# Performance work log

Hardware: AMD Instinct MI355X
Metric: run time of the kernel (lower is better)

Reference implementation:

```python
import jax, jax.numpy as jnp
import numpy as np

B, T, C, D = 4, 2048, 1024, 64

def setup_inputs() -> dict:
    key = jax.random.key(0)
    ks = jax.random.split(key, 7)
    s = 1.0 / np.sqrt(C)
    return {
        "x":  jax.random.normal(ks[0], (B, T, C), dtype=jnp.float32),
        "Wq": jax.random.uniform(ks[1], (C, D), jnp.float32, -s, s),
        "bq": jax.random.uniform(ks[2], (D,),  jnp.float32, -s, s),
        "Wk": jax.random.uniform(ks[3], (C, D), jnp.float32, -s, s),
        "bk": jax.random.uniform(ks[4], (D,),  jnp.float32, -s, s),
        "Wv": jax.random.uniform(ks[5], (C, D), jnp.float32, -s, s),
        "bv": jax.random.uniform(ks[6], (D,),  jnp.float32, -s, s),
    }

def reference(x, Wq, bq, Wk, bk, Wv, bv):
    # QKV projections: [B,T,C] @ [C,D] -> [B,T,D]
    Q = jnp.einsum('btc,cd->btd', x, Wq) + bq
    K = jnp.einsum('btc,cd->btd', x, Wk) + bk
    V = jnp.einsum('btc,cd->btd', x, Wv) + bv
    scale = 1.0 / jnp.sqrt(jnp.float32(D))
    wei = jnp.einsum('bqd,bkd->bqk', Q, K) * scale  # [B,T,T]
    causal = jnp.tril(jnp.ones((T, T), dtype=bool))
    wei = jnp.where(causal, wei, jnp.float32(-1e9))  # masked_fill, not -inf
    wei = jax.nn.softmax(wei, axis=-1)
    return jnp.einsum('bqk,bkd->bqd', wei, V)  # [B,T,D]
```

## Files before the change

### kernel.cpp

```cpp
#include <hip/hip_runtime.h>
#include <stdint.h>

#define B_  4
#define T_  2048
#define C_  1024
#define D_  64

typedef float  f32x4  __attribute__((ext_vector_type(4)));
typedef float  f32x16 __attribute__((ext_vector_type(16)));
typedef short  s16x8  __attribute__((ext_vector_type(8)));

#define QSCALE 0.18033688011112042f

static __device__ __forceinline__ uint32_t f2bf(float f) {
  uint32_t u = __builtin_bit_cast(uint32_t, f);
  u += 0x7FFFu + ((u >> 16) & 1u);
  return u >> 16;
}
static __device__ __forceinline__ uint32_t pack2bf(float a, float b) {
  return f2bf(a) | (f2bf(b) << 16);
}

__global__ __launch_bounds__(256) void wconv_kernel(
    const float* __restrict__ Wq, const float* __restrict__ bq,
    const float* __restrict__ Wk, const float* __restrict__ bk,
    const float* __restrict__ Wv, const float* __restrict__ bv,
    uint16_t* __restrict__ Wp, float* __restrict__ biascat) {
  const int g = blockIdx.x * 256 + threadIdx.x;
  const int s32   = g / 768;
  const int rem   = g - s32 * 768;
  const int ntile = rem >> 6;
  const int l     = rem & 63;
  const int mrow  = l & 15, u = l >> 4;
  const int n     = ntile * 16 + mrow;
  const int mat   = n >> 6, col = n & 63;
  const float* W  = (mat == 0) ? Wq : ((mat == 1) ? Wk : Wv);
  const float  s  = (mat == 0) ? QSCALE : 1.0f;
  const int c0    = s32 * 32 + u * 8;
  float v[8];
#pragma unroll
  for (int j = 0; j < 8; ++j) v[j] = W[(size_t)(c0 + j) * D_ + col] * s;
  uint4 st;
  st.x = pack2bf(v[0], v[1]);
  st.y = pack2bf(v[2], v[3]);
  st.z = pack2bf(v[4], v[5]);
  st.w = pack2bf(v[6], v[7]);
  *reinterpret_cast<uint4*>(Wp + (size_t)g * 8) = st;
  if (g < 192) {
    float bb;
    if (g < 64)       bb = bq[g] * QSCALE;
    else if (g < 128) bb = bk[g - 64];
    else              bb = bv[g - 128];
    biascat[g] = bb;
  }
}

__global__ __launch_bounds__(512) void proj_kernel(
    const float* __restrict__ x, const uint16_t* __restrict__ Wp,
    const float* __restrict__ biascat,
    uint16_t* __restrict__ Qfrag, uint16_t* __restrict__ Kfrag,
    uint16_t* __restrict__ Vfrag) {
  __shared__ __align__(16) uint16_t xt[2][32 * 132];
  __shared__ __align__(16) uint16_t tbuf[8][16 * 28];
  const int tid   = threadIdx.x;
  const int wave  = tid >> 6;
  const int lane  = tid & 63;
  const int mrow  = lane & 15;
  const int u     = lane >> 4;
  const int wn    = wave & 3;
  const int mhalf = wave >> 2;
  const int m0    = blockIdx.x * 32;
  const int mw    = m0 + mhalf * 16;
  const int srow  = tid >> 4, scol = tid & 15;

  const float* xg = x + (size_t)(m0 + srow) * C_ + scol * 4;

  f32x4 acc[3];
#pragma unroll
  for (int i = 0; i < 3; ++i)
#pragma unroll
    for (int r = 0; r < 4; ++r) acc[i][r] = 0.f;

  float4 xv0 = *reinterpret_cast<const float4*>(xg);
  float4 xv1 = *reinterpret_cast<const float4*>(xg + 64);
  {
    uint2 w0, w1;
    w0.x = pack2bf(xv0.x, xv0.y);  w0.y = pack2bf(xv0.z, xv0.w);
    w1.x = pack2bf(xv1.x, xv1.y);  w1.y = pack2bf(xv1.z, xv1.w);
    *reinterpret_cast<uint2*>(&xt[0][srow * 132 + scol * 4])      = w0;
    *reinterpret_cast<uint2*>(&xt[0][srow * 132 + scol * 4 + 64]) = w1;
  }
  __syncthreads();

  for (int s = 0; s < 8; ++s) {
    const int cur = s & 1;
    if (s < 7) {
      xv0 = *reinterpret_cast<const float4*>(xg + (s + 1) * 128);
      xv1 = *reinterpret_cast<const float4*>(xg + (s + 1) * 128 + 64);
    }
#pragma unroll
    for (int step = 0; step < 4; ++step) {
      const int s32 = s * 4 + step;
      s16x8 bf = *reinterpret_cast<const s16x8*>(
          &xt[cur][(mhalf * 16 + mrow) * 132 + step * 32 + u * 8]);
      const uint16_t* wb = Wp + ((size_t)(s32 * 12 + wn * 3) * 64 + lane) * 8;
      s16x8 a0 = *reinterpret_cast<const s16x8*>(wb);
      s16x8 a1 = *reinterpret_cast<const s16x8*>(wb + 64 * 8);
      s16x8 a2 = *reinterpret_cast<const s16x8*>(wb + 128 * 8);
      acc[0] = __builtin_amdgcn_mfma_f32_16x16x32_bf16(a0, bf, acc[0], 0, 0, 0);
      acc[1] = __builtin_amdgcn_mfma_f32_16x16x32_bf16(a1, bf, acc[1], 0, 0, 0);
      acc[2] = __builtin_amdgcn_mfma_f32_16x16x32_bf16(a2, bf, acc[2], 0, 0, 0);
    }
    if (s < 7) {
      uint2 w0, w1;
      w0.x = pack2bf(xv0.x, xv0.y);  w0.y = pack2bf(xv0.z, xv0.w);
      w1.x = pack2bf(xv1.x, xv1.y);  w1.y = pack2bf(xv1.z, xv1.w);
      *reinterpret_cast<uint2*>(&xt[cur ^ 1][srow * 132 + scol * 4])      = w0;
      *reinterpret_cast<uint2*>(&xt[cur ^ 1][srow * 132 + scol * 4 + 64]) = w1;
      __syncthreads();
    }
  }

  const int bb = m0 >> 11;
  const int mm = mw & (T_ - 1);
#pragma unroll
  for (int nt = 0; nt < 3; ++nt) {
    const int nb = wn * 48 + nt * 16;
    uint16_t vals[4];
#pragma unroll
    for (int r = 0; r < 4; ++r)
      vals[r] = (uint16_t)f2bf(acc[nt][r] + biascat[nb + u * 4 + r]);
    if (nb >= 128) {
      const int tg  = mm + mrow;
      const int t   = tg >> 5, rem = tg & 31;
      const int kc  = rem >> 4, hi2 = (rem >> 3) & 1, jj = rem & 7;
      uint16_t* base = Vfrag + ((size_t)(bb * 64 + t)) * 2048;
#pragma unroll
      for (int r = 0; r < 4; ++r) {
        int d = nb - 128 + u * 4 + r;
        int i = (d >> 5) * 2 + kc;
        int l = hi2 * 32 + (d & 31);
        base[i * 512 + l * 8 + jj] = vals[r];
      }
    } else {
#pragma unroll
      for (int r = 0; r < 4; ++r)
        tbuf[wave][mrow * 28 + u * 4 + r] = vals[r];
      const int row = lane >> 2, qtr = lane & 3;
      uint2 v = *reinterpret_cast<const uint2*>(&tbuf[wave][row * 28 + qtr * 4]);
      const int m  = mw + row;
      const int e0 = (nb & 63) + qtr * 4;
      const int t  = (m & 2047) >> 5;
      const int c  = e0 >> 4, hi2 = (e0 >> 3) & 1, j0 = e0 & 7;
      uint16_t* dst = (nb < 64) ? Qfrag : Kfrag;
      *reinterpret_cast<uint2*>(
          dst + ((size_t)(bb * 64 + t)) * 2048 + c * 512 +
          (hi2 * 32 + (m & 31)) * 8 + j0) = v;
    }
  }
}

__global__ __launch_bounds__(512) void attn_kernel(
    const uint16_t* __restrict__ Qfrag, const uint16_t* __restrict__ Kfrag,
    const uint16_t* __restrict__ Vfrag, float* __restrict__ out) {
  __shared__ float wpart[8 * 2048];
  __shared__ float lw[8 * 32];
  __shared__ float lbuf[32];

  const int tid  = threadIdx.x;
  const int wave = tid >> 6;
  const int lane = tid & 63;
  const int ql   = lane & 31;
  const int hi   = lane >> 5;

  const int blk = blockIdx.x;
  const int b   = blk & 3;
  const int qt  = 63 - (blk >> 2);

  s16x8 qf[4];
  {
    const uint16_t* qg = Qfrag + ((size_t)(b * 64 + qt)) * 2048 + lane * 8;
#pragma unroll
    for (int c = 0; c < 4; ++c)
      qf[c] = *reinterpret_cast<const s16x8*>(qg + c * 512);
  }

  f32x16 aco[2];
#pragma unroll
  for (int i = 0; i < 2; ++i)
#pragma unroll
    for (int r = 0; r < 16; ++r) aco[i][r] = 0.f;
  float lacc = 0.f;

  auto load_tile = [&](int t, s16x8* kf, s16x8* vf) {
    const uint16_t* kg = Kfrag + ((size_t)(b * 64 + t)) * 2048 + lane * 8;
#pragma unroll
    for (int c = 0; c < 4; ++c)
      kf[c] = *reinterpret_cast<const s16x8*>(kg + c * 512);
    const uint16_t* vg = Vfrag + ((size_t)(b * 64 + t)) * 2048 + lane * 8;
#pragma unroll
    for (int i = 0; i < 4; ++i)
      vf[i] = *reinterpret_cast<const s16x8*>(vg + i * 512);
  };

  auto compute = [&](int t, const s16x8* kf, const s16x8* vf) {
    f32x16 sacc;
#pragma unroll
    for (int r = 0; r < 16; ++r) sacc[r] = 0.f;
#pragma unroll
    for (int c = 0; c < 4; ++c)
      sacc = __builtin_amdgcn_mfma_f32_32x32x16_bf16(kf[c], qf[c], sacc, 0, 0, 0);
    if (t == qt) {
#pragma unroll
      for (int r = 0; r < 16; ++r) {
        const int koff = (r & 3) + 8 * (r >> 2) + 4 * hi;
        sacc[r] = (koff > ql) ? -1e30f : sacc[r];
      }
    }
    float p[16];
#pragma unroll
    for (int r = 0; r < 16; ++r) p[r] = __builtin_amdgcn_exp2f(sacc[r]);
    float s01 = (p[0] + p[1]) + (p[2] + p[3]);
    float s23 = (p[4] + p[5]) + (p[6] + p[7]);
    float s45 = (p[8] + p[9]) + (p[10] + p[11]);
    float s67 = (p[12] + p[13]) + (p[14] + p[15]);
    lacc += (s01 + s23) + (s45 + s67);

    uint32_t A0 = pack2bf(p[0], p[1]),  A1 = pack2bf(p[2], p[3]);
    uint32_t B0 = pack2bf(p[4], p[5]),  B1 = pack2bf(p[6], p[7]);
    uint32_t C0 = pack2bf(p[8], p[9]),  C1 = pack2bf(p[10], p[11]);
    uint32_t D0 = pack2bf(p[12], p[13]), D1 = pack2bf(p[14], p[15]);
    uint32_t r0 = (uint32_t)__shfl_xor((int)(hi ? A0 : B0), 32, 64);
    uint32_t r1 = (uint32_t)__shfl_xor((int)(hi ? A1 : B1), 32, 64);
    uint32_t r2 = (uint32_t)__shfl_xor((int)(hi ? C0 : D0), 32, 64);
    uint32_t r3 = (uint32_t)__shfl_xor((int)(hi ? C1 : D1), 32, 64);
    union { uint32_t u[4]; s16x8 v; } pf0, pf1;
    pf0.u[0] = hi ? r0 : A0;  pf0.u[1] = hi ? r1 : A1;
    pf0.u[2] = hi ? B0 : r0;  pf0.u[3] = hi ? B1 : r1;
    pf1.u[0] = hi ? r2 : C0;  pf1.u[1] = hi ? r3 : C1;
    pf1.u[2] = hi ? D0 : r2;  pf1.u[3] = hi ? D1 : r3;
    aco[0] = __builtin_amdgcn_mfma_f32_32x32x16_bf16(vf[0], pf0.v, aco[0], 0, 0, 0);
    aco[1] = __builtin_amdgcn_mfma_f32_32x32x16_bf16(vf[2], pf0.v, aco[1], 0, 0, 0);
    aco[0] = __builtin_amdgcn_mfma_f32_32x32x16_bf16(vf[1], pf1.v, aco[0], 0, 0, 0);
    aco[1] = __builtin_amdgcn_mfma_f32_32x32x16_bf16(vf[3], pf1.v, aco[1], 0, 0, 0);
  };

  {
    int t = wave;
    if (t <= qt) {
      s16x8 kfA[4], vfA[4], kfB[4], vfB[4];
      load_tile(t, kfA, vfA);
      while (true) {
        int tn = t + 8;
        if (tn <= qt) load_tile(tn, kfB, vfB);
        compute(t, kfA, vfA);
        if (tn > qt) break;
        t = tn; tn = t + 8;
        if (tn <= qt) load_tile(tn, kfA, vfA);
        compute(t, kfB, vfB);
        if (tn > qt) break;
        t = tn;
      }
    }
  }

  lacc += __shfl_xor(lacc, 32, 64);

#pragma unroll
  for (int dm = 0; dm < 2; ++dm)
#pragma unroll
    for (int r = 0; r < 16; ++r)
      wpart[wave * 2048 + dm * 1024 + r * 64 + hi * 32 + ql] = aco[dm][r];
  if (hi == 0) lw[wave * 32 + ql] = lacc;
  __syncthreads();

  const int base = tid * 4;
  float4 s0 = {0.f, 0.f, 0.f, 0.f};
#pragma unroll
  for (int w = 0; w < 8; ++w) {
    float4 a = *reinterpret_cast<const float4*>(wpart + w * 2048 + base);
    s0.x += a.x; s0.y += a.y; s0.z += a.z; s0.w += a.w;
  }
  if (tid < 32) {
    float ls = 0.f;
#pragma unroll
    for (int w = 0; w < 8; ++w) ls += lw[w * 32 + tid];
    lbuf[tid] = 1.0f / ls;
  }
  __syncthreads();

  float* trans = wpart;
  {
    const int dm = base >> 10, r = (base >> 6) & 15, h2 = (base >> 5) & 1;
    const int ql0 = base & 31;
    const int d = dm * 32 + (r & 3) + 8 * (r >> 2) + 4 * h2;
    float* tr = &trans[d * 33 + ql0];
    tr[0] = s0.x; tr[1] = s0.y; tr[2] = s0.z; tr[3] = s0.w;
  }
  __syncthreads();

  {
    const int q  = tid >> 4;
    const int dg = (tid & 15) * 4;
    const float rinv = lbuf[q];
    float4 o;
    o.x = trans[(dg + 0) * 33 + q] * rinv;
    o.y = trans[(dg + 1) * 33 + q] * rinv;
    o.z = trans[(dg + 2) * 33 + q] * rinv;
    o.w = trans[(dg + 3) * 33 + q] * rinv;
    *reinterpret_cast<float4*>(
        out + ((size_t)(b * T_ + qt * 32 + q)) * D_ + dg) = o;
  }
}

extern "C" void kernel_launch(void* const* d_in, const int* in_sizes, int n_in,
                              void* d_out, int out_size, void* d_ws, size_t ws_size,
                              hipStream_t stream) {
  (void)in_sizes; (void)n_in; (void)out_size; (void)ws_size;
  const float* x  = (const float*)d_in[0];
  const float* Wq = (const float*)d_in[1];
  const float* bq = (const float*)d_in[2];
  const float* Wk = (const float*)d_in[3];
  const float* bk = (const float*)d_in[4];
  const float* Wv = (const float*)d_in[5];
  const float* bv = (const float*)d_in[6];
  float* out = (float*)d_out;

  char* ws = (char*)d_ws;
  uint16_t* Wp      = (uint16_t*)(ws);
  float*    biascat = (float*)(ws + 393216);
  uint16_t* Qfrag   = (uint16_t*)(ws + 394240);
  uint16_t* Kfrag   = (uint16_t*)(ws + 1442816);
  uint16_t* Vfrag   = (uint16_t*)(ws + 2491392);

  hipLaunchKernelGGL(wconv_kernel, dim3(96), dim3(256), 0, stream,
                     Wq, bq, Wk, bk, Wv, bv, Wp, biascat);
  hipLaunchKernelGGL(proj_kernel, dim3(256), dim3(512), 0, stream,
                     x, Wp, biascat, Qfrag, Kfrag, Vfrag);
  hipLaunchKernelGGL(attn_kernel, dim3(256), dim3(512), 0, stream,
                     Qfrag, Kfrag, Vfrag, out);
}
```

Measured before the change: 102.2 us.

## Fuse weight conversion, projection and attention into one cooperative kernel

Merges the three kernels into a single cooperative launch that separates the weight-conversion, projection and attention phases with grid-wide syncs. Shared memory is one raw buffer reused by each phase. The aim is to remove two kernel launch gaps and their tail drain. In exchange every block now carries the larger shared-memory footprint and pays for grid barriers. The three-kernel path is kept as a fallback if the cooperative launch fails.

```diff
diff --git a/kernel.cpp b/kernel.cpp
--- a/kernel.cpp
+++ b/kernel.cpp
@@ -1,5 +1,8 @@
 #include <hip/hip_runtime.h>
+#include <hip/hip_cooperative_groups.h>
 #include <stdint.h>
+
+namespace cg = cooperative_groups;
 
 #define B_  4
 #define T_  2048
@@ -21,12 +24,14 @@
   return f2bf(a) | (f2bf(b) << 16);
 }
 
-__global__ __launch_bounds__(256) void wconv_kernel(
+
+static __device__ __forceinline__ void wconv_body(
+    int g,
     const float* __restrict__ Wq, const float* __restrict__ bq,
     const float* __restrict__ Wk, const float* __restrict__ bk,
     const float* __restrict__ Wv, const float* __restrict__ bv,
     uint16_t* __restrict__ Wp, float* __restrict__ biascat) {
-  const int g = blockIdx.x * 256 + threadIdx.x;
+  if (g >= 24576) return;
   const int s32   = g / 768;
   const int rem   = g - s32 * 768;
   const int ntile = rem >> 6;
@@ -55,21 +60,21 @@
   }
 }
 
-__global__ __launch_bounds__(512) void proj_kernel(
+static __device__ __forceinline__ void proj_body(
+    int bx, int tid, char* smem,
     const float* __restrict__ x, const uint16_t* __restrict__ Wp,
     const float* __restrict__ biascat,
     uint16_t* __restrict__ Qfrag, uint16_t* __restrict__ Kfrag,
     uint16_t* __restrict__ Vfrag) {
-  __shared__ __align__(16) uint16_t xt[2][32 * 132];
-  __shared__ __align__(16) uint16_t tbuf[8][16 * 28];
-  const int tid   = threadIdx.x;
+  uint16_t* xt   = (uint16_t*)smem;
+  uint16_t* tbuf = (uint16_t*)(smem + 16896);
   const int wave  = tid >> 6;
   const int lane  = tid & 63;
   const int mrow  = lane & 15;
   const int u     = lane >> 4;
   const int wn    = wave & 3;
   const int mhalf = wave >> 2;
-  const int m0    = blockIdx.x * 32;
+  const int m0    = bx * 32;
   const int mw    = m0 + mhalf * 16;
   const int srow  = tid >> 4, scol = tid & 15;
 
@@ -87,8 +92,8 @@
     uint2 w0, w1;
     w0.x = pack2bf(xv0.x, xv0.y);  w0.y = pack2bf(xv0.z, xv0.w);
     w1.x = pack2bf(xv1.x, xv1.y);  w1.y = pack2bf(xv1.z, xv1.w);
-    *reinterpret_cast<uint2*>(&xt[0][srow * 132 + scol * 4])      = w0;
-    *reinterpret_cast<uint2*>(&xt[0][srow * 132 + scol * 4 + 64]) = w1;
+    *reinterpret_cast<uint2*>(&xt[srow * 132 + scol * 4])      = w0;
+    *reinterpret_cast<uint2*>(&xt[srow * 132 + scol * 4 + 64]) = w1;
   }
   __syncthreads();
 
@@ -102,7 +107,7 @@
     for (int step = 0; step < 4; ++step) {
       const int s32 = s * 4 + step;
       s16x8 bf = *reinterpret_cast<const s16x8*>(
-          &xt[cur][(mhalf * 16 + mrow) * 132 + step * 32 + u * 8]);
+          &xt[cur * 4224 + (mhalf * 16 + mrow) * 132 + step * 32 + u * 8]);
       const uint16_t* wb = Wp + ((size_t)(s32 * 12 + wn * 3) * 64 + lane) * 8;
       s16x8 a0 = *reinterpret_cast<const s16x8*>(wb);
       s16x8 a1 = *reinterpret_cast<const s16x8*>(wb + 64 * 8);
@@ -115,8 +120,8 @@
       uint2 w0, w1;
       w0.x = pack2bf(xv0.x, xv0.y);  w0.y = pack2bf(xv0.z, xv0.w);
       w1.x = pack2bf(xv1.x, xv1.y);  w1.y = pack2bf(xv1.z, xv1.w);
-      *reinterpret_cast<uint2*>(&xt[cur ^ 1][srow * 132 + scol * 4])      = w0;
-      *reinterpret_cast<uint2*>(&xt[cur ^ 1][srow * 132 + scol * 4 + 64]) = w1;
+      *reinterpret_cast<uint2*>(&xt[(cur ^ 1) * 4224 + srow * 132 + scol * 4])      = w0;
+      *reinterpret_cast<uint2*>(&xt[(cur ^ 1) * 4224 + srow * 132 + scol * 4 + 64]) = w1;
       __syncthreads();
     }
   }
@@ -145,9 +150,10 @@
     } else {
 #pragma unroll
       for (int r = 0; r < 4; ++r)
-        tbuf[wave][mrow * 28 + u * 4 + r] = vals[r];
+        tbuf[wave * 448 + mrow * 28 + u * 4 + r] = vals[r];
       const int row = lane >> 2, qtr = lane & 3;
-      uint2 v = *reinterpret_cast<const uint2*>(&tbuf[wave][row * 28 + qtr * 4]);
+      uint2 v = *reinterpret_cast<const uint2*>(
+          &tbuf[wave * 448 + row * 28 + qtr * 4]);
       const int m  = mw + row;
       const int e0 = (nb & 63) + qtr * 4;
       const int t  = (m & 2047) >> 5;
@@ -160,22 +166,21 @@
   }
 }
 
-__global__ __launch_bounds__(512) void attn_kernel(
+static __device__ __forceinline__ void attn_body(
+    int bx, int tid, char* smem,
     const uint16_t* __restrict__ Qfrag, const uint16_t* __restrict__ Kfrag,
     const uint16_t* __restrict__ Vfrag, float* __restrict__ out) {
-  __shared__ float wpart[8 * 2048];
-  __shared__ float lw[8 * 32];
-  __shared__ float lbuf[32];
-
-  const int tid  = threadIdx.x;
+  float* wpart = (float*)smem;
+  float* lw    = (float*)(smem + 65536);
+  float* lbuf  = (float*)(smem + 66560);
+
   const int wave = tid >> 6;
   const int lane = tid & 63;
   const int ql   = lane & 31;
   const int hi   = lane >> 5;
 
-  const int blk = blockIdx.x;
-  const int b   = blk & 3;
-  const int qt  = 63 - (blk >> 2);
+  const int b   = bx & 3;
+  const int qt  = 63 - (bx >> 2);
 
   s16x8 qf[4];
   {
@@ -313,6 +318,55 @@
   }
 }
 
+__global__ __launch_bounds__(512) void fused_kernel(
+    const float* __restrict__ x,
+    const float* __restrict__ Wq, const float* __restrict__ bq,
+    const float* __restrict__ Wk, const float* __restrict__ bk,
+    const float* __restrict__ Wv, const float* __restrict__ bv,
+    float* __restrict__ out,
+    uint16_t* __restrict__ Wp, float* __restrict__ biascat,
+    uint16_t* __restrict__ Qfrag, uint16_t* __restrict__ Kfrag,
+    uint16_t* __restrict__ Vfrag) {
+  cg::grid_group grid = cg::this_grid();
+  __shared__ __align__(16) char smem[66688];
+  const int tid = threadIdx.x;
+  const int bx  = blockIdx.x;
+
+  wconv_body(bx * 512 + tid, Wq, bq, Wk, bk, Wv, bv, Wp, biascat);
+  __threadfence();
+  grid.sync();
+
+  proj_body(bx, tid, smem, x, Wp, biascat, Qfrag, Kfrag, Vfrag);
+  __threadfence();
+  grid.sync();
+
+  attn_body(bx, tid, smem, Qfrag, Kfrag, Vfrag, out);
+}
+
+__global__ __launch_bounds__(256) void wconv_kernel(
+    const float* __restrict__ Wq, const float* __restrict__ bq,
+    const float* __restrict__ Wk, const float* __restrict__ bk,
+    const float* __restrict__ Wv, const float* __restrict__ bv,
+    uint16_t* __restrict__ Wp, float* __restrict__ biascat) {
+  wconv_body(blockIdx.x * 256 + threadIdx.x, Wq, bq, Wk, bk, Wv, bv, Wp, biascat);
+}
+
+__global__ __launch_bounds__(512) void proj_kernel(
+    const float* __restrict__ x, const uint16_t* __restrict__ Wp,
+    const float* __restrict__ biascat,
+    uint16_t* __restrict__ Qfrag, uint16_t* __restrict__ Kfrag,
+    uint16_t* __restrict__ Vfrag) {
+  __shared__ __align__(16) char smem[24064];
+  proj_body(blockIdx.x, threadIdx.x, smem, x, Wp, biascat, Qfrag, Kfrag, Vfrag);
+}
+
+__global__ __launch_bounds__(512) void attn_kernel(
+    const uint16_t* __restrict__ Qfrag, const uint16_t* __restrict__ Kfrag,
+    const uint16_t* __restrict__ Vfrag, float* __restrict__ out) {
+  __shared__ __align__(16) char smem[66688];
+  attn_body(blockIdx.x, threadIdx.x, smem, Qfrag, Kfrag, Vfrag, out);
+}
+
 extern "C" void kernel_launch(void* const* d_in, const int* in_sizes, int n_in,
                               void* d_out, int out_size, void* d_ws, size_t ws_size,
                               hipStream_t stream) {
@@ -333,10 +387,20 @@
   uint16_t* Kfrag   = (uint16_t*)(ws + 1442816);
   uint16_t* Vfrag   = (uint16_t*)(ws + 2491392);
 
-  hipLaunchKernelGGL(wconv_kernel, dim3(96), dim3(256), 0, stream,
-                     Wq, bq, Wk, bk, Wv, bv, Wp, biascat);
-  hipLaunchKernelGGL(proj_kernel, dim3(256), dim3(512), 0, stream,
-                     x, Wp, biascat, Qfrag, Kfrag, Vfrag);
-  hipLaunchKernelGGL(attn_kernel, dim3(256), dim3(512), 0, stream,
-                     Qfrag, Kfrag, Vfrag, out);
-}
+  void* kargs[] = {
+    (void*)&x, (void*)&Wq, (void*)&bq, (void*)&Wk, (void*)&bk,
+    (void*)&Wv, (void*)&bv, (void*)&out, (void*)&Wp, (void*)&biascat,
+    (void*)&Qfrag, (void*)&Kfrag, (void*)&Vfrag
+  };
+  hipError_t err = hipLaunchCooperativeKernel(
+      (const void*)fused_kernel, dim3(256), dim3(512), kargs, 0, stream);
+  if (err != hipSuccess) {
+    (void)hipGetLastError();
+    hipLaunchKernelGGL(wconv_kernel, dim3(96), dim3(256), 0, stream,
+                       Wq, bq, Wk, bk, Wv, bv, Wp, biascat);
+    hipLaunchKernelGGL(proj_kernel, dim3(256), dim3(512), 0, stream,
+                       x, Wp, biascat, Qfrag, Kfrag, Vfrag);
+    hipLaunchKernelGGL(attn_kernel, dim3(256), dim3(512), 0, stream,
+                       Qfrag, Kfrag, Vfrag, out);
+  }
+}
```

After: 271.8 us. 2.66x slower.
